# Kernel optimization log

Measured on AMD Instinct MI355X. Metric: run time of the kernel, lower is better.

## Reference

```python
import jax, jax.numpy as jnp
import numpy as np

B, S, T = 512, 1024, 48  # batch, seq_len, num_tags


def setup_inputs() -> dict:
    key = jax.random.key(0)
    k1, k2, k3, k4, k5, k6 = jax.random.split(key, 6)
    emissions = jax.random.normal(k1, (B, S, T), dtype=jnp.float32)
    tags = jax.random.randint(k2, (B, S), 0, T)
    lengths = jax.random.randint(k3, (B,), 1, S + 1)
    mask = jnp.arange(S)[None, :] < lengths[:, None]  # contiguous prefix mask, bool
    # learned parameters (nn.Parameter zeros init in the module; use small random here)
    start_transitions = 0.01 * jax.random.normal(k4, (T,), dtype=jnp.float32)
    end_transitions = 0.01 * jax.random.normal(k5, (T,), dtype=jnp.float32)
    transitions = 0.01 * jax.random.normal(k6, (T, T), dtype=jnp.float32)
    return {
        "emissions": emissions,
        "tags": tags,
        "mask": mask,
        "start_transitions": start_transitions,
        "end_transitions": end_transitions,
        "transitions": transitions,
    }


def _log_partition(emissions, mask, start_transitions, end_transitions, transitions):
    # score[b, i] = log-sum over paths ending in tag i (note: this repo indexes
    # transitions[i, j] with j = previous tag inside the partition recursion).
    score0 = start_transitions[None, :] + emissions[:, 0]  # (B, T)

    def step(score, xs):
        emit_t, mask_t = xs  # (B, T), (B,)
        # score_t[b, i] = logsumexp_j(score[b, j] + transitions[i, j]) + emit_t[b, i]
        score_t = jax.nn.logsumexp(score[:, None, :] + transitions[None, :, :], axis=2) + emit_t
        score = jnp.where(mask_t[:, None], score_t, score)
        return score, None

    em = jnp.swapaxes(emissions[:, 1:], 0, 1)  # (S-1, B, T)
    mk = jnp.swapaxes(mask[:, 1:], 0, 1)       # (S-1, B)
    score, _ = jax.lax.scan(step, score0, (em, mk))
    return jax.nn.logsumexp(score + end_transitions[None, :], axis=1)  # (B,)


def _score_sentence(emissions, tags, mask, start_transitions, end_transitions, transitions):
    Bb = emissions.shape[0]
    bidx = jnp.arange(Bb)
    maskf = mask.astype(emissions.dtype)
    score = start_transitions[tags[:, 0]] + emissions[bidx, 0, tags[:, 0]]  # (B,)
    trans_sc = transitions[tags[:, :-1], tags[:, 1:]]  # (B, S-1)
    emit_sc = jnp.take_along_axis(emissions, tags[:, :, None], axis=2)[..., 0]  # (B, S)
    score = score + jnp.sum((trans_sc + emit_sc[:, 1:]) * maskf[:, 1:], axis=1)
    last_idx = jnp.sum(mask.astype(jnp.int32), axis=1) - 1  # (B,)
    last_tags = jnp.take_along_axis(tags, last_idx[:, None], axis=1)[:, 0]
    return score + end_transitions[last_tags]


def reference(emissions, tags, mask, start_transitions, end_transitions, transitions):
    log_denominator = _log_partition(emissions, mask, start_transitions, end_transitions, transitions)
    log_numerator = _score_sentence(emissions, tags, mask, start_transitions, end_transitions, transitions)
    return jnp.mean(log_denominator - log_numerator)
```

## Files before the change

kernel.cpp:

```cpp
#include <hip/hip_runtime.h>

#define BB 512
#define SS 1024
#define TT 48
#define GG 16
#define CK 8
#define NSLOT 5

typedef __attribute__((ext_vector_type(8))) short short8;
typedef __attribute__((ext_vector_type(4))) float float4v;

__device__ __forceinline__ unsigned short f2bf(float x) {
    unsigned u = __float_as_uint(x);
    u += 0x7FFFu + ((u >> 16) & 1u);
    return (unsigned short)(u >> 16);
}
__device__ __forceinline__ unsigned pk2bf(float lo, float hi) {
#if __has_builtin(__builtin_amdgcn_cvt_pk_bf16_f32)
    typedef __bf16 bf16x2 __attribute__((ext_vector_type(2)));
    union { bf16x2 v; unsigned u; } cv;
    cv.v = __builtin_amdgcn_cvt_pk_bf16_f32(lo, hi);
    return cv.u;
#else
    return __builtin_amdgcn_perm(__float_as_uint(hi) + 0x8000u,
                                 __float_as_uint(lo) + 0x8000u, 0x07060302u);
#endif
}
__device__ __forceinline__ float bflo(unsigned u) { return __uint_as_float(u << 16); }
__device__ __forceinline__ float bfhi(unsigned u) { return __uint_as_float(u & 0xFFFF0000u); }
__device__ __forceinline__ float wave_sum(float v) {
#pragma unroll
    for (int off = 32; off >= 1; off >>= 1) v += __shfl_xor(v, off, 64);
    return v;
}
__device__ __forceinline__ int wave_sum_i(int v) {
#pragma unroll
    for (int off = 32; off >= 1; off >>= 1) v += __shfl_xor(v, off, 64);
    return v;
}

__global__ __launch_bounds__(256)
void crf_numer(const float* __restrict__ em, const int* __restrict__ tags,
               const int* __restrict__ mask, const float* __restrict__ start_tr,
               const float* __restrict__ end_tr, const float* __restrict__ trans,
               float* __restrict__ numer, int* __restrict__ lenArr) {
    const int b = blockIdx.x, tid = threadIdx.x;
    const float* emb = em + (size_t)b * SS * TT;
    const int* tg = tags + (size_t)b * SS;
    const int* mk = mask + (size_t)b * SS;
    int cnt = 0; float ns = 0.f;
    for (int s = tid; s < SS; s += 256) {
        int m = mk[s];
        cnt += (m != 0);
        if (s >= 1 && m) {
            int tp = tg[s - 1], tc = tg[s];
            ns += trans[tp * TT + tc] + emb[s * TT + tc];
        }
    }
    float wsum = wave_sum(ns);
    int wcnt = wave_sum_i(cnt);
    __shared__ float sf[4]; __shared__ int si[4];
    if ((tid & 63) == 0) { sf[tid >> 6] = wsum; si[tid >> 6] = wcnt; }
    __syncthreads();
    if (tid == 0) {
        float tot = sf[0] + sf[1] + sf[2] + sf[3];
        int L = si[0] + si[1] + si[2] + si[3];
        int t0 = tg[0];
        tot += start_tr[t0] + emb[t0] + end_tr[tg[L - 1]];
        numer[b] = tot;
        lenArr[b] = L;
    }
}

__global__ __launch_bounds__(320, 1)
void crf_fwd(const float* __restrict__ em, const float* __restrict__ start_tr,
             const float* __restrict__ end_tr, const float* __restrict__ trans,
             const int* __restrict__ lenArr, float* __restrict__ denomArr) {
    __shared__ uint2 ring[NSLOT * CK * 3 * 64];

    const int tid = threadIdx.x;
    const int wave = tid >> 6, lane = tid & 63;
    const int wgbase = blockIdx.x * GG;

    if (wave == 0) {
        const int n = lane & 15, q = lane >> 4;
        const int bb = wgbase + n;

        short8 afr[3][2];
#pragma unroll
        for (int mt = 0; mt < 3; ++mt) {
            const int so = mt * 16 + n;
#pragma unroll
            for (int kt = 0; kt < 2; ++kt) {
                short8 a;
#pragma unroll
                for (int i = 0; i < 8; ++i) {
                    int si_;
                    if (kt == 0) si_ = (i < 4) ? (q * 4 + i) : (16 + q * 4 + (i - 4));
                    else         si_ = (i < 4) ? (32 + q * 4 + i) : -1;
                    a[i] = (si_ >= 0) ? (short)f2bf(__expf(trans[so * TT + si_])) : (short)0;
                }
                afr[mt][kt] = a;
            }
        }

        const float* em0 = em + (size_t)bb * SS * TT + q * 4;
        float p[3][4];
#pragma unroll
        for (int mt = 0; mt < 3; ++mt) {
            float4 v = *(const float4*)(em0 + mt * 16);
            int sb = mt * 16 + q * 4;
            p[mt][0] = __expf(start_tr[sb + 0] + v.x);
            p[mt][1] = __expf(start_tr[sb + 1] + v.y);
            p[mt][2] = __expf(start_tr[sb + 2] + v.z);
            p[mt][3] = __expf(start_tr[sb + 3] + v.w);
        }

        const int len = lenArr[bb];
        int Lmax = len;
#pragma unroll
        for (int off = 1; off < 64; off <<= 1) {
            int o = __shfl_xor(Lmax, off, 64);
            Lmax = Lmax > o ? Lmax : o;
        }
        const int P = (Lmax + 6) >> 3;

        bool cc0 = (len == 1);
        float dc[3][4];
#pragma unroll
        for (int mt = 0; mt < 3; ++mt)
#pragma unroll
            for (int r = 0; r < 4; ++r) dc[mt][r] = cc0 ? p[mt][r] : 0.f;
        float lcap = 0.f, logscale = 0.f;
        const float4v Z = {0.f, 0.f, 0.f, 0.f};

        for (int pp = -3; pp < P; ++pp) {
            if (pp >= 0) {
                const uint2* rp = &ring[(pp % NSLOT) * (CK * 3 * 64) + lane];
                uint2 c0 = rp[0], c1 = rp[64], c2v = rp[128];
#pragma unroll
                for (int u = 0; u < 8; ++u) {
                    uint2 n0, n1, n2;
                    if (u < 7) {
                        n0 = rp[(u + 1) * 192];
                        n1 = rp[(u + 1) * 192 + 64];
                        n2 = rp[(u + 1) * 192 + 128];
                    }
                    union { short8 v; unsigned w[4]; } B0, B1;
                    B0.w[0] = pk2bf(p[0][0], p[0][1]); B0.w[1] = pk2bf(p[0][2], p[0][3]);
                    B0.w[2] = pk2bf(p[1][0], p[1][1]); B0.w[3] = pk2bf(p[1][2], p[1][3]);
                    B1.w[0] = pk2bf(p[2][0], p[2][1]); B1.w[1] = pk2bf(p[2][2], p[2][3]);
                    B1.w[2] = 0u; B1.w[3] = 0u;
                    float4v A0 = __builtin_amdgcn_mfma_f32_16x16x32_bf16(afr[0][0], B0.v, Z, 0, 0, 0);
                    float4v A1 = __builtin_amdgcn_mfma_f32_16x16x32_bf16(afr[1][0], B0.v, Z, 0, 0, 0);
                    float4v A2 = __builtin_amdgcn_mfma_f32_16x16x32_bf16(afr[2][0], B0.v, Z, 0, 0, 0);
                    A0 = __builtin_amdgcn_mfma_f32_16x16x32_bf16(afr[0][1], B1.v, A0, 0, 0, 0);
                    A1 = __builtin_amdgcn_mfma_f32_16x16x32_bf16(afr[1][1], B1.v, A1, 0, 0, 0);
                    A2 = __builtin_amdgcn_mfma_f32_16x16x32_bf16(afr[2][1], B1.v, A2, 0, 0, 0);
                    p[0][0] = A0[0] * bflo(c0.x); p[0][1] = A0[1] * bfhi(c0.x);
                    p[0][2] = A0[2] * bflo(c0.y); p[0][3] = A0[3] * bfhi(c0.y);
                    p[1][0] = A1[0] * bflo(c1.x); p[1][1] = A1[1] * bfhi(c1.x);
                    p[1][2] = A1[2] * bflo(c1.y); p[1][3] = A1[3] * bfhi(c1.y);
                    p[2][0] = A2[0] * bflo(c2v.x); p[2][1] = A2[1] * bfhi(c2v.x);
                    p[2][2] = A2[2] * bflo(c2v.y); p[2][3] = A2[3] * bfhi(c2v.y);
                    bool cc = (len == 8 * pp + u + 2);
#pragma unroll
                    for (int mt = 0; mt < 3; ++mt)
#pragma unroll
                        for (int r = 0; r < 4; ++r) dc[mt][r] = cc ? p[mt][r] : dc[mt][r];
                    lcap = cc ? logscale : lcap;
                    c0 = n0; c1 = n1; c2v = n2;
                    if (u == 7) {
                        float m = fmaxf(p[0][0], p[0][1]);
                        m = fmaxf(m, fmaxf(p[0][2], p[0][3]));
                        m = fmaxf(m, fmaxf(p[1][0], p[1][1]));
                        m = fmaxf(m, fmaxf(p[1][2], p[1][3]));
                        m = fmaxf(m, fmaxf(p[2][0], p[2][1]));
                        m = fmaxf(m, fmaxf(p[2][2], p[2][3]));
                        m = fmaxf(m, __shfl_xor(m, 16, 64));
                        m = fmaxf(m, __shfl_xor(m, 32, 64));
                        m = fmaxf(m, 1e-30f);
                        logscale += __logf(m);
                        float rm = __builtin_amdgcn_rcpf(m);
#pragma unroll
                        for (int mt = 0; mt < 3; ++mt)
#pragma unroll
                            for (int r = 0; r < 4; ++r) p[mt][r] *= rm;
                    }
                }
            }
            __builtin_amdgcn_s_barrier();
        }

        float pe = 0.f;
#pragma unroll
        for (int mt = 0; mt < 3; ++mt) {
            int sb = mt * 16 + q * 4;
            pe = fmaf(dc[mt][0], __expf(end_tr[sb + 0]), pe);
            pe = fmaf(dc[mt][1], __expf(end_tr[sb + 1]), pe);
            pe = fmaf(dc[mt][2], __expf(end_tr[sb + 2]), pe);
            pe = fmaf(dc[mt][3], __expf(end_tr[sb + 3]), pe);
        }
        pe += __shfl_xor(pe, 16, 64);
        pe += __shfl_xor(pe, 32, 64);
        if (lane < 16) denomArr[bb] = lcap + __logf(pe);

    } else {
        const int T = (wave - 1) >> 1;
        const int sub = (wave - 1) & 1;
        const int nb = lane & 15, q4 = lane >> 4;
        const int bb = wgbase + nb;
        const int len_v = lenArr[bb];
        int Lmax = len_v;
#pragma unroll
        for (int off = 1; off < 64; off <<= 1) {
            int o = __shfl_xor(Lmax, off, 64);
            Lmax = Lmax > o ? Lmax : o;
        }
        const int P = (Lmax + 6) >> 3;

        const float* emP = em + (size_t)bb * SS * TT + q4 * 4;
        float4 buf[12];

        for (int pp = -3; pp < P; ++pp) {
            int cv = pp + 1;
            if (cv >= 0 && cv < P && (cv & 1) == T) {
                uint2* wp = &ring[(cv % NSLOT) * (CK * 3 * 64) + lane];
#pragma unroll
                for (int k = 0; k < 12; ++k) {
                    const int i = sub * 12 + k, u = i / 3, j = i % 3;
                    int t = 1 + 8 * cv + u;
                    bool live = t < len_v;
                    float4 v = buf[k];
                    unsigned ox = pk2bf(__expf(v.x), __expf(v.y));
                    unsigned oy = pk2bf(__expf(v.z), __expf(v.w));
                    uint2 o;
                    o.x = live ? ox : 0u;
                    o.y = live ? oy : 0u;
                    wp[u * 192 + j * 64] = o;
                }
            }
            int ci = pp + 3;
            if (ci < P && (ci & 1) == T) {
#pragma unroll
                for (int k = 0; k < 12; ++k) {
                    const int i = sub * 12 + k, u = i / 3, j = i % 3;
                    int t = 1 + 8 * ci + u; t = t < SS ? t : SS - 1;
                    buf[k] = *(const float4*)(emP + (size_t)t * TT + j * 16);
                }
            }
            __builtin_amdgcn_s_waitcnt(0xC07F);
            __builtin_amdgcn_s_barrier();
        }
    }
}

__global__ __launch_bounds__(64)
void crf_reduce(const float* __restrict__ denom, const float* __restrict__ numer,
                float* __restrict__ out) {
    int lane = threadIdx.x;
    float s = 0.f;
    for (int i = lane; i < BB; i += 64) s += denom[i] - numer[i];
    s = wave_sum(s);
    if (lane == 0) out[0] = s * (1.0f / (float)BB);
}

extern "C" void kernel_launch(void* const* d_in, const int* in_sizes, int n_in,
                              void* d_out, int out_size, void* d_ws, size_t ws_size,
                              hipStream_t stream) {
    const float* emissions = (const float*)d_in[0];
    const int*   tags      = (const int*)d_in[1];
    const int*   mask      = (const int*)d_in[2];
    const float* start_tr  = (const float*)d_in[3];
    const float* end_tr    = (const float*)d_in[4];
    const float* trans     = (const float*)d_in[5];

    char* ws = (char*)d_ws;
    float* denom = (float*)ws;
    float* numer = (float*)(ws + 2048);
    int*   lenA  = (int*)(ws + 4096);

    crf_numer<<<BB, 256, 0, stream>>>(emissions, tags, mask, start_tr, end_tr,
                                      trans, numer, lenA);
    crf_fwd<<<BB / GG, 320, 0, stream>>>(emissions, start_tr, end_tr, trans,
                                         lenA, denom);
    crf_reduce<<<1, 64, 0, stream>>>(denom, numer, (float*)d_out);
}
```

Before: 321.6 us.

## Split forward recursion into parallel sequence chunks with matrix products

Replaces the serial per-batch forward scan with a chunked scheme. Each wave computes the 48x48 product of scaled transition matrices over a 128-step chunk using MFMA, and a combine kernel then chains the eight chunk matrices per sequence. This exposes parallelism along the sequence to remove the long serial latency chain. In exchange it does three times the MFMA work per step, writes and reads about 37 MB of intermediate matrices, and adds an extra launch.

Result: no change. 327.0 us (+1.7%).

```diff
diff --git a/kernel.cpp b/kernel.cpp
--- a/kernel.cpp
+++ b/kernel.cpp
@@ -3,9 +3,8 @@
 #define BB 512
 #define SS 1024
 #define TT 48
-#define GG 16
-#define CK 8
-#define NSLOT 5
+#define CH 8
+#define CL 128
 
 typedef __attribute__((ext_vector_type(8))) short short8;
 typedef __attribute__((ext_vector_type(4))) float float4v;
@@ -26,8 +25,6 @@
                                  __float_as_uint(lo) + 0x8000u, 0x07060302u);
 #endif
 }
-__device__ __forceinline__ float bflo(unsigned u) { return __uint_as_float(u << 16); }
-__device__ __forceinline__ float bfhi(unsigned u) { return __uint_as_float(u & 0xFFFF0000u); }
 __device__ __forceinline__ float wave_sum(float v) {
 #pragma unroll
     for (int off = 32; off >= 1; off >>= 1) v += __shfl_xor(v, off, 64);
@@ -72,187 +69,206 @@
     }
 }
 
-__global__ __launch_bounds__(320, 1)
-void crf_fwd(const float* __restrict__ em, const float* __restrict__ start_tr,
-             const float* __restrict__ end_tr, const float* __restrict__ trans,
-             const int* __restrict__ lenArr, float* __restrict__ denomArr) {
-    __shared__ uint2 ring[NSLOT * CK * 3 * 64];
-
-    const int tid = threadIdx.x;
-    const int wave = tid >> 6, lane = tid & 63;
-    const int wgbase = blockIdx.x * GG;
-
-    if (wave == 0) {
-        const int n = lane & 15, q = lane >> 4;
-        const int bb = wgbase + n;
-
-        short8 afr[3][2];
-#pragma unroll
-        for (int mt = 0; mt < 3; ++mt) {
-            const int so = mt * 16 + n;
-#pragma unroll
-            for (int kt = 0; kt < 2; ++kt) {
-                short8 a;
-#pragma unroll
-                for (int i = 0; i < 8; ++i) {
-                    int si_;
-                    if (kt == 0) si_ = (i < 4) ? (q * 4 + i) : (16 + q * 4 + (i - 4));
-                    else         si_ = (i < 4) ? (32 + q * 4 + i) : -1;
-                    a[i] = (si_ >= 0) ? (short)f2bf(__expf(trans[so * TT + si_])) : (short)0;
-                }
-                afr[mt][kt] = a;
+__global__ __launch_bounds__(256, 1)
+void crf_chunk(const float* __restrict__ em, const float* __restrict__ trans,
+               const int* __restrict__ lenArr, float* __restrict__ Mout,
+               float* __restrict__ scaleOut) {
+    const int wid = blockIdx.x * 4 + (threadIdx.x >> 6);
+    const int lane = threadIdx.x & 63;
+    const int b = wid >> 3, c = wid & 7;
+    const int n = lane & 15, q = lane >> 4;
+
+    const int len = lenArr[b];
+    const int t0 = 1 + c * CL;
+    int t1 = t0 + CL; if (t1 > len) t1 = len;
+    float* MO = Mout + (size_t)wid * (TT * TT);
+
+    if (t1 <= t0) {
+#pragma unroll
+        for (int mt = 0; mt < 3; ++mt)
+#pragma unroll
+            for (int r = 0; r < 4; ++r) {
+                int row = mt * 16 + q * 4 + r;
+#pragma unroll
+                for (int nt = 0; nt < 3; ++nt)
+                    MO[row * TT + nt * 16 + n] = (row == nt * 16 + n) ? 1.0f : 0.0f;
             }
-        }
-
-        const float* em0 = em + (size_t)bb * SS * TT + q * 4;
-        float p[3][4];
-#pragma unroll
-        for (int mt = 0; mt < 3; ++mt) {
-            float4 v = *(const float4*)(em0 + mt * 16);
-            int sb = mt * 16 + q * 4;
-            p[mt][0] = __expf(start_tr[sb + 0] + v.x);
-            p[mt][1] = __expf(start_tr[sb + 1] + v.y);
-            p[mt][2] = __expf(start_tr[sb + 2] + v.z);
-            p[mt][3] = __expf(start_tr[sb + 3] + v.w);
-        }
-
-        const int len = lenArr[bb];
-        int Lmax = len;
-#pragma unroll
-        for (int off = 1; off < 64; off <<= 1) {
-            int o = __shfl_xor(Lmax, off, 64);
-            Lmax = Lmax > o ? Lmax : o;
-        }
-        const int P = (Lmax + 6) >> 3;
-
-        bool cc0 = (len == 1);
-        float dc[3][4];
-#pragma unroll
-        for (int mt = 0; mt < 3; ++mt)
-#pragma unroll
-            for (int r = 0; r < 4; ++r) dc[mt][r] = cc0 ? p[mt][r] : 0.f;
-        float lcap = 0.f, logscale = 0.f;
-        const float4v Z = {0.f, 0.f, 0.f, 0.f};
-
-        for (int pp = -3; pp < P; ++pp) {
-            if (pp >= 0) {
-                const uint2* rp = &ring[(pp % NSLOT) * (CK * 3 * 64) + lane];
-                uint2 c0 = rp[0], c1 = rp[64], c2v = rp[128];
-#pragma unroll
-                for (int u = 0; u < 8; ++u) {
-                    uint2 n0, n1, n2;
-                    if (u < 7) {
-                        n0 = rp[(u + 1) * 192];
-                        n1 = rp[(u + 1) * 192 + 64];
-                        n2 = rp[(u + 1) * 192 + 128];
-                    }
-                    union { short8 v; unsigned w[4]; } B0, B1;
-                    B0.w[0] = pk2bf(p[0][0], p[0][1]); B0.w[1] = pk2bf(p[0][2], p[0][3]);
-                    B0.w[2] = pk2bf(p[1][0], p[1][1]); B0.w[3] = pk2bf(p[1][2], p[1][3]);
-                    B1.w[0] = pk2bf(p[2][0], p[2][1]); B1.w[1] = pk2bf(p[2][2], p[2][3]);
-                    B1.w[2] = 0u; B1.w[3] = 0u;
-                    float4v A0 = __builtin_amdgcn_mfma_f32_16x16x32_bf16(afr[0][0], B0.v, Z, 0, 0, 0);
-                    float4v A1 = __builtin_amdgcn_mfma_f32_16x16x32_bf16(afr[1][0], B0.v, Z, 0, 0, 0);
-                    float4v A2 = __builtin_amdgcn_mfma_f32_16x16x32_bf16(afr[2][0], B0.v, Z, 0, 0, 0);
-                    A0 = __builtin_amdgcn_mfma_f32_16x16x32_bf16(afr[0][1], B1.v, A0, 0, 0, 0);
-                    A1 = __builtin_amdgcn_mfma_f32_16x16x32_bf16(afr[1][1], B1.v, A1, 0, 0, 0);
-                    A2 = __builtin_amdgcn_mfma_f32_16x16x32_bf16(afr[2][1], B1.v, A2, 0, 0, 0);
-                    p[0][0] = A0[0] * bflo(c0.x); p[0][1] = A0[1] * bfhi(c0.x);
-                    p[0][2] = A0[2] * bflo(c0.y); p[0][3] = A0[3] * bfhi(c0.y);
-                    p[1][0] = A1[0] * bflo(c1.x); p[1][1] = A1[1] * bfhi(c1.x);
-                    p[1][2] = A1[2] * bflo(c1.y); p[1][3] = A1[3] * bfhi(c1.y);
-                    p[2][0] = A2[0] * bflo(c2v.x); p[2][1] = A2[1] * bfhi(c2v.x);
-                    p[2][2] = A2[2] * bflo(c2v.y); p[2][3] = A2[3] * bfhi(c2v.y);
-                    bool cc = (len == 8 * pp + u + 2);
-#pragma unroll
-                    for (int mt = 0; mt < 3; ++mt)
-#pragma unroll
-                        for (int r = 0; r < 4; ++r) dc[mt][r] = cc ? p[mt][r] : dc[mt][r];
-                    lcap = cc ? logscale : lcap;
-                    c0 = n0; c1 = n1; c2v = n2;
-                    if (u == 7) {
-                        float m = fmaxf(p[0][0], p[0][1]);
-                        m = fmaxf(m, fmaxf(p[0][2], p[0][3]));
-                        m = fmaxf(m, fmaxf(p[1][0], p[1][1]));
-                        m = fmaxf(m, fmaxf(p[1][2], p[1][3]));
-                        m = fmaxf(m, fmaxf(p[2][0], p[2][1]));
-                        m = fmaxf(m, fmaxf(p[2][2], p[2][3]));
-                        m = fmaxf(m, __shfl_xor(m, 16, 64));
-                        m = fmaxf(m, __shfl_xor(m, 32, 64));
-                        m = fmaxf(m, 1e-30f);
-                        logscale += __logf(m);
-                        float rm = __builtin_amdgcn_rcpf(m);
-#pragma unroll
-                        for (int mt = 0; mt < 3; ++mt)
-#pragma unroll
-                            for (int r = 0; r < 4; ++r) p[mt][r] *= rm;
-                    }
-                }
+        if (lane == 0) scaleOut[wid] = 0.f;
+        return;
+    }
+
+    short8 afr[3][2];
+#pragma unroll
+    for (int mt = 0; mt < 3; ++mt) {
+        const int so = mt * 16 + n;
+#pragma unroll
+        for (int kt = 0; kt < 2; ++kt) {
+            short8 a;
+#pragma unroll
+            for (int i = 0; i < 8; ++i) {
+                int si_;
+                if (kt == 0) si_ = (i < 4) ? (q * 4 + i) : (16 + q * 4 + (i - 4));
+                else         si_ = (i < 4) ? (32 + q * 4 + i) : -1;
+                a[i] = (si_ >= 0) ? (short)f2bf(__expf(trans[so * TT + si_])) : (short)0;
             }
-            __builtin_amdgcn_s_barrier();
-        }
-
-        float pe = 0.f;
-#pragma unroll
-        for (int mt = 0; mt < 3; ++mt) {
-            int sb = mt * 16 + q * 4;
-            pe = fmaf(dc[mt][0], __expf(end_tr[sb + 0]), pe);
-            pe = fmaf(dc[mt][1], __expf(end_tr[sb + 1]), pe);
-            pe = fmaf(dc[mt][2], __expf(end_tr[sb + 2]), pe);
-            pe = fmaf(dc[mt][3], __expf(end_tr[sb + 3]), pe);
-        }
-        pe += __shfl_xor(pe, 16, 64);
-        pe += __shfl_xor(pe, 32, 64);
-        if (lane < 16) denomArr[bb] = lcap + __logf(pe);
-
-    } else {
-        const int T = (wave - 1) >> 1;
-        const int sub = (wave - 1) & 1;
-        const int nb = lane & 15, q4 = lane >> 4;
-        const int bb = wgbase + nb;
-        const int len_v = lenArr[bb];
-        int Lmax = len_v;
-#pragma unroll
-        for (int off = 1; off < 64; off <<= 1) {
-            int o = __shfl_xor(Lmax, off, 64);
-            Lmax = Lmax > o ? Lmax : o;
-        }
-        const int P = (Lmax + 6) >> 3;
-
-        const float* emP = em + (size_t)bb * SS * TT + q4 * 4;
-        float4 buf[12];
-
-        for (int pp = -3; pp < P; ++pp) {
-            int cv = pp + 1;
-            if (cv >= 0 && cv < P && (cv & 1) == T) {
-                uint2* wp = &ring[(cv % NSLOT) * (CK * 3 * 64) + lane];
-#pragma unroll
-                for (int k = 0; k < 12; ++k) {
-                    const int i = sub * 12 + k, u = i / 3, j = i % 3;
-                    int t = 1 + 8 * cv + u;
-                    bool live = t < len_v;
-                    float4 v = buf[k];
-                    unsigned ox = pk2bf(__expf(v.x), __expf(v.y));
-                    unsigned oy = pk2bf(__expf(v.z), __expf(v.w));
-                    uint2 o;
-                    o.x = live ? ox : 0u;
-                    o.y = live ? oy : 0u;
-                    wp[u * 192 + j * 64] = o;
-                }
+            afr[mt][kt] = a;
+        }
+    }
+
+    float C[3][3][4];
+#pragma unroll
+    for (int mt = 0; mt < 3; ++mt)
+#pragma unroll
+        for (int nt = 0; nt < 3; ++nt)
+#pragma unroll
+            for (int r = 0; r < 4; ++r)
+                C[mt][nt][r] = (mt == nt && n == q * 4 + r) ? 1.0f : 0.0f;
+
+    int badr[12];
+#pragma unroll
+    for (int mt = 0; mt < 3; ++mt)
+#pragma unroll
+        for (int r = 0; r < 4; ++r)
+            badr[mt * 4 + r] = 4 * (mt * 16 + q * 4 + r);
+
+    const float* ep = em + (size_t)b * SS * TT + (lane & 47);
+    float logscale = 0.f;
+    const float4v Zv = {0.f, 0.f, 0.f, 0.f};
+
+#define CSTEP(EV) {                                                                    \
+    union { short8 v; unsigned w[4]; } B0[3], B1[3];                                   \
+    _Pragma("unroll")                                                                  \
+    for (int nt = 0; nt < 3; ++nt) {                                                   \
+        B0[nt].w[0] = pk2bf(C[0][nt][0], C[0][nt][1]);                                 \
+        B0[nt].w[1] = pk2bf(C[0][nt][2], C[0][nt][3]);                                 \
+        B0[nt].w[2] = pk2bf(C[1][nt][0], C[1][nt][1]);                                 \
+        B0[nt].w[3] = pk2bf(C[1][nt][2], C[1][nt][3]);                                 \
+        B1[nt].w[0] = pk2bf(C[2][nt][0], C[2][nt][1]);                                 \
+        B1[nt].w[1] = pk2bf(C[2][nt][2], C[2][nt][3]);                                 \
+        B1[nt].w[2] = 0u; B1[nt].w[3] = 0u;                                            \
+    }                                                                                  \
+    float ee = __expf(EV);                                                             \
+    float er[12];                                                                      \
+    _Pragma("unroll")                                                                  \
+    for (int i = 0; i < 12; ++i)                                                       \
+        er[i] = __uint_as_float(__builtin_amdgcn_ds_bpermute(badr[i], __float_as_int(ee))); \
+    _Pragma("unroll")                                                                  \
+    for (int mt = 0; mt < 3; ++mt) {                                                   \
+        _Pragma("unroll")                                                              \
+        for (int nt = 0; nt < 3; ++nt) {                                               \
+            float4v D = __builtin_amdgcn_mfma_f32_16x16x32_bf16(afr[mt][0], B0[nt].v, Zv, 0, 0, 0); \
+            D = __builtin_amdgcn_mfma_f32_16x16x32_bf16(afr[mt][1], B1[nt].v, D, 0, 0, 0);          \
+            C[mt][nt][0] = D[0] * er[mt * 4 + 0];                                      \
+            C[mt][nt][1] = D[1] * er[mt * 4 + 1];                                      \
+            C[mt][nt][2] = D[2] * er[mt * 4 + 2];                                      \
+            C[mt][nt][3] = D[3] * er[mt * 4 + 3];                                      \
+        }                                                                              \
+    }                                                                                  \
+}
+
+#define CRENORM {                                                                      \
+    float m_ = C[0][0][0];                                                             \
+    _Pragma("unroll") for (int mt = 0; mt < 3; ++mt)                                   \
+    _Pragma("unroll") for (int nt = 0; nt < 3; ++nt)                                   \
+    _Pragma("unroll") for (int r = 0; r < 4; ++r) m_ = fmaxf(m_, C[mt][nt][r]);        \
+    _Pragma("unroll") for (int off = 1; off < 64; off <<= 1)                           \
+        m_ = fmaxf(m_, __shfl_xor(m_, off, 64));                                       \
+    m_ = fmaxf(m_, 1e-30f);                                                            \
+    logscale += __logf(m_);                                                            \
+    float rm_ = 1.0f / m_;                                                             \
+    _Pragma("unroll") for (int mt = 0; mt < 3; ++mt)                                   \
+    _Pragma("unroll") for (int nt = 0; nt < 3; ++nt)                                   \
+    _Pragma("unroll") for (int r = 0; r < 4; ++r) C[mt][nt][r] *= rm_;                 \
+}
+
+    float ea[8], eb[8];
+#pragma unroll
+    for (int k = 0; k < 8; ++k) {
+        int tt = t0 + k; tt = tt < t1 ? tt : t1 - 1;
+        ea[k] = ep[(size_t)tt * TT];
+    }
+    int t = t0;
+    for (; t + 16 <= t1; t += 16) {
+#pragma unroll
+        for (int k = 0; k < 8; ++k) eb[k] = ep[(size_t)(t + 8 + k) * TT];
+        CSTEP(ea[0]) CSTEP(ea[1]) CSTEP(ea[2]) CSTEP(ea[3])
+        CSTEP(ea[4]) CSTEP(ea[5]) CSTEP(ea[6]) CSTEP(ea[7])
+        CRENORM
+#pragma unroll
+        for (int k = 0; k < 8; ++k) {
+            int tt = t + 16 + k; tt = tt < t1 ? tt : t1 - 1;
+            ea[k] = ep[(size_t)tt * TT];
+        }
+        CSTEP(eb[0]) CSTEP(eb[1]) CSTEP(eb[2]) CSTEP(eb[3])
+        CSTEP(eb[4]) CSTEP(eb[5]) CSTEP(eb[6]) CSTEP(eb[7])
+        CRENORM
+    }
+    int rem = t1 - t;
+#pragma unroll
+    for (int k = 0; k < 8; ++k) { if (k < rem) CSTEP(ea[k]) }
+    CRENORM
+    if (rem > 8) {
+#pragma unroll
+        for (int k = 0; k < 8; ++k) {
+            int tt = t + 8 + k; tt = tt < t1 ? tt : t1 - 1;
+            eb[k] = ep[(size_t)tt * TT];
+        }
+#pragma unroll
+        for (int k = 0; k < 8; ++k) { if (k + 8 < rem) CSTEP(eb[k]) }
+        CRENORM
+    }
+
+#pragma unroll
+    for (int mt = 0; mt < 3; ++mt)
+#pragma unroll
+        for (int r = 0; r < 4; ++r) {
+            int row = mt * 16 + q * 4 + r;
+#pragma unroll
+            for (int nt = 0; nt < 3; ++nt)
+                MO[row * TT + nt * 16 + n] = C[mt][nt][r];
+        }
+    if (lane == 0) scaleOut[wid] = logscale;
+#undef CSTEP
+#undef CRENORM
+}
+
+__global__ __launch_bounds__(64)
+void crf_comb(const float* __restrict__ em, const float* __restrict__ start_tr,
+              const float* __restrict__ end_tr, const float* __restrict__ Mall,
+              const float* __restrict__ scaleAll, float* __restrict__ denomArr) {
+    const int b = blockIdx.x, lane = threadIdx.x;
+    __shared__ float pl[TT];
+    float p = 0.f;
+    if (lane < TT) p = __expf(start_tr[lane] + em[(size_t)b * SS * TT + lane]);
+    float logscale = 0.f;
+#pragma unroll 1
+    for (int c = 0; c < CH; ++c) {
+        if (lane < TT) pl[lane] = p;
+        __syncthreads();
+        const float* M = Mall + ((size_t)(b * CH + c)) * (TT * TT) + lane * TT;
+        float acc = 0.f;
+        if (lane < TT) {
+#pragma unroll
+            for (int j = 0; j < TT; j += 4) {
+                float4 m4 = *(const float4*)(M + j);
+                acc = fmaf(m4.x, pl[j], acc);
+                acc = fmaf(m4.y, pl[j + 1], acc);
+                acc = fmaf(m4.z, pl[j + 2], acc);
+                acc = fmaf(m4.w, pl[j + 3], acc);
             }
-            int ci = pp + 3;
-            if (ci < P && (ci & 1) == T) {
-#pragma unroll
-                for (int k = 0; k < 12; ++k) {
-                    const int i = sub * 12 + k, u = i / 3, j = i % 3;
-                    int t = 1 + 8 * ci + u; t = t < SS ? t : SS - 1;
-                    buf[k] = *(const float4*)(emP + (size_t)t * TT + j * 16);
-                }
-            }
-            __builtin_amdgcn_s_waitcnt(0xC07F);
-            __builtin_amdgcn_s_barrier();
-        }
-    }
+        }
+        logscale += scaleAll[b * CH + c];
+        float mm = acc;
+#pragma unroll
+        for (int off = 1; off < 64; off <<= 1) mm = fmaxf(mm, __shfl_xor(mm, off, 64));
+        mm = fmaxf(mm, 1e-30f);
+        logscale += __logf(mm);
+        p = acc * (1.0f / mm);
+        __syncthreads();
+    }
+    float pe = (lane < TT) ? p * __expf(end_tr[lane]) : 0.f;
+    pe = wave_sum(pe);
+    if (lane == 0) denomArr[b] = logscale + __logf(pe);
 }
 
 __global__ __launch_bounds__(64)
@@ -276,13 +292,16 @@
     const float* trans     = (const float*)d_in[5];
 
     char* ws = (char*)d_ws;
-    float* denom = (float*)ws;
-    float* numer = (float*)(ws + 2048);
-    int*   lenA  = (int*)(ws + 4096);
+    const size_t MF_BYTES = (size_t)BB * CH * TT * TT * 4;
+    float* MF     = (float*)ws;
+    float* scaleA = (float*)(ws + MF_BYTES);
+    float* denom  = (float*)(ws + MF_BYTES + 16384);
+    float* numer  = (float*)(ws + MF_BYTES + 18432);
+    int*   lenA   = (int*)(ws + MF_BYTES + 20480);
 
     crf_numer<<<BB, 256, 0, stream>>>(emissions, tags, mask, start_tr, end_tr,
                                       trans, numer, lenA);
-    crf_fwd<<<BB / GG, 320, 0, stream>>>(emissions, start_tr, end_tr, trans,
-                                         lenA, denom);
+    crf_chunk<<<BB * CH / 4, 256, 0, stream>>>(emissions, trans, lenA, MF, scaleA);
+    crf_comb<<<BB, 64, 0, stream>>>(emissions, start_tr, end_tr, MF, scaleA, denom);
     crf_reduce<<<1, 64, 0, stream>>>(denom, numer, (float*)d_out);
 }
```
